# Performance work log

Hardware: AMD Instinct MI355X
Metric: run time of the kernel (lower is better)

The kernel has to match this reference:

```python
import jax, jax.numpy as jnp
import numpy as np


def setup_inputs() -> dict:
    key = jax.random.key(0)
    k1, k2 = jax.random.split(key)
    B, C, H, W, K = 8, 32, 224, 224, 5
    x = jax.random.normal(k1, (B, C, H, W), dtype=jnp.float32)
    kernel = jax.random.normal(k2, (C, 1, K, K), dtype=jnp.float32) * 0.1
    return {"x": x, "kernel": kernel, "stride": 1, "padding": 2, "dilation": 1}


def reference(x, kernel, stride, padding, dilation):
    # Tropical-max (morphological dilation) conv: out[p] = max_k (x[p+k] + w_flipped[k]).
    # is_max=True, softmax_temp=None -> hard max; kernel is flipped (true convolution).
    B, C, H, W = x.shape
    OC, _, K, _ = kernel.shape
    neutral = -jnp.inf
    x_pad = jnp.pad(x, ((0, 0), (0, 0), (padding, padding), (padding, padding)),
                    constant_values=neutral)
    Hp, Wp = H + 2 * padding, W + 2 * padding
    H_out = (Hp - dilation * (K - 1) - 1) // stride + 1
    W_out = (Wp - dilation * (K - 1) - 1) // stride + 1
    wflip = kernel[:, 0, ::-1, ::-1]  # (C, K, K) flipped, as in torch kernel.flip((2,3))
    # Start from neutral: matches the extra neutral row padded onto the unfold tensor.
    out = jnp.full((B, C, H_out, W_out), neutral, dtype=x.dtype)
    for i in range(K):  # small fixed K*K loop; avoids materializing the (B,C,K^2,HW) unfold
        for j in range(K):
            patch = x_pad[:, :,
                          i * dilation: i * dilation + (H_out - 1) * stride + 1: stride,
                          j * dilation: j * dilation + (W_out - 1) * stride + 1: stride]
            out = jnp.maximum(out, patch + wflip[:, i, j][None, :, None, None])
    return out
```

## Files before the change

### kernel.cpp

```cpp
#include <hip/hip_runtime.h>
#include <math.h>


#define TC_B 8
#define TC_C 32
#define TC_H 224
#define TC_W 224
#define TC_WQ (TC_W / 4)
#define TC_HG (TC_H / 16)
#define T_ROWS 20
#define T_STRIDE 240
#define T_F4_PER_ROW 56

__global__ __launch_bounds__(256) void tropical_conv2d_kernel(
    const float* __restrict__ x, const float* __restrict__ kern,
    float* __restrict__ out) {
  const int wq = threadIdx.x;
  const int hl = threadIdx.y;
  const int blk = blockIdx.x;
  const int hg = blk % TC_HG;
  const int bc = blk / TC_HG;
  const int c = bc % TC_C;

  __shared__ float tile[T_ROWS * T_STRIDE];

  const float NEG = -INFINITY;
  const float4 NINF4 = make_float4(NEG, NEG, NEG, NEG);
  const int t = hl * 64 + wq;
  const int row0 = hg * 16 - 2;
  const float* xp = x + (size_t)bc * (TC_H * TC_W);

  if (t < 40) {
    const int r = t % T_ROWS;
    const int cf = (t < T_ROWS) ? 0 : 57;
    *(float4*)&tile[r * T_STRIDE + cf * 4] = NINF4;
  }

  #pragma unroll
  for (int k = 0; k < 5; ++k) {
    const int idx = t + k * 256;
    if (idx < T_ROWS * T_F4_PER_ROW) {
      const int r = idx / T_F4_PER_ROW;
      const int cf = idx % T_F4_PER_ROW;
      const int ir = row0 + r;
      float4 val;
      if (ir >= 0 && ir < TC_H)
        val = ((const float4*)(xp + (size_t)ir * TC_W))[cf];
      else
        val = NINF4;
      *(float4*)&tile[r * T_STRIDE + (1 + cf) * 4] = val;
    }
  }

  float w[25];
  #pragma unroll
  for (int q = 0; q < 25; ++q) w[q] = kern[c * 25 + 24 - q];

  __syncthreads();

  if (wq >= TC_WQ) return;

  float acc[4][4];
  #pragma unroll
  for (int o = 0; o < 4; ++o)
    #pragma unroll
    for (int k = 0; k < 4; ++k) acc[o][k] = NEG;

  #pragma unroll
  for (int ri = 0; ri < 8; ++ri) {
    const float* rp = &tile[(hl * 4 + ri) * T_STRIDE + 4 * wq];
    const float4 A = *(const float4*)(rp);
    const float4 Bv = *(const float4*)(rp + 4);
    const float4 Cv = *(const float4*)(rp + 8);
    float v[12] = {A.x, A.y, A.z, A.w, Bv.x, Bv.y, Bv.z, Bv.w,
                   Cv.x, Cv.y, Cv.z, Cv.w};

    #pragma unroll
    for (int o = 0; o < 4; ++o) {
      const int i = ri - o;
      if (i < 0 || i > 4) continue;
      #pragma unroll
      for (int k = 0; k < 4; ++k) {
        const float t0 = v[2 + k + 0] + w[i * 5 + 0];
        const float t1 = v[2 + k + 1] + w[i * 5 + 1];
        const float t2 = v[2 + k + 2] + w[i * 5 + 2];
        const float t3 = v[2 + k + 3] + w[i * 5 + 3];
        const float t4 = v[2 + k + 4] + w[i * 5 + 4];
        acc[o][k] = fmaxf(fmaxf(fmaxf(acc[o][k], t0), t1),
                          fmaxf(fmaxf(t2, t3), t4));
      }
    }
  }

  float* op = out + (size_t)bc * (TC_H * TC_W) + (size_t)(hg * 16 + hl * 4) * TC_W;
  #pragma unroll
  for (int o = 0; o < 4; ++o) {
    ((float4*)(op + (size_t)o * TC_W))[wq] =
        make_float4(acc[o][0], acc[o][1], acc[o][2], acc[o][3]);
  }
}

extern "C" void kernel_launch(void* const* d_in, const int* in_sizes, int n_in,
                              void* d_out, int out_size, void* d_ws, size_t ws_size,
                              hipStream_t stream) {
  const float* x = (const float*)d_in[0];
  const float* k = (const float*)d_in[1];
  float* out = (float*)d_out;

  dim3 block(64, 4, 1);
  dim3 grid(TC_B * TC_C * TC_HG, 1, 1);
  tropical_conv2d_kernel<<<grid, block, 0, stream>>>(x, k, out);
}
```

Before: 114.8 us.

## Loop over row tiles per block with register-prefetched global loads

Each block now covers a quarter of an image plane (56 rows) instead of 16 rows. It walks four row tiles, prefetching the next tile's global data into registers while computing the current tile from shared memory. Blocks grow to 512 threads, with each thread producing 2 output rows instead of 4. The aim is to hide global load latency and amortise block launch and weight loads. In exchange there are fewer blocks, two barriers per tile, and more shared-memory reads per output.

After: 146.8 us. 27.9% more time.

```diff
diff --git a/kernel.cpp b/kernel.cpp
--- a/kernel.cpp
+++ b/kernel.cpp
@@ -6,97 +6,119 @@
 #define TC_C 32
 #define TC_H 224
 #define TC_W 224
-#define TC_WQ (TC_W / 4)
-#define TC_HG (TC_H / 16)
+#define TC_WQ 56
+#define T_STRIDE 232
 #define T_ROWS 20
-#define T_STRIDE 240
-#define T_F4_PER_ROW 56
+#define N_TILES 4
+#define QROWS 56
 
-__global__ __launch_bounds__(256) void tropical_conv2d_kernel(
+__global__ __launch_bounds__(512) void tropical_conv2d_kernel(
     const float* __restrict__ x, const float* __restrict__ kern,
     float* __restrict__ out) {
-  const int wq = threadIdx.x;
-  const int hl = threadIdx.y;
+  const int tt = threadIdx.x;
+  const int wq = tt & 63;
+  const int yl = tt >> 6;
   const int blk = blockIdx.x;
-  const int hg = blk % TC_HG;
-  const int bc = blk / TC_HG;
-  const int c = bc % TC_C;
+  const int hq = blk & 3;
+  const int bc = blk >> 2;
+  const int c = bc & (TC_C - 1);
+  const int h0 = hq * QROWS;
 
   __shared__ float tile[T_ROWS * T_STRIDE];
 
   const float NEG = -INFINITY;
   const float4 NINF4 = make_float4(NEG, NEG, NEG, NEG);
-  const int t = hl * 64 + wq;
-  const int row0 = hg * 16 - 2;
-  const float* xp = x + (size_t)bc * (TC_H * TC_W);
 
-  if (t < 40) {
-    const int r = t % T_ROWS;
-    const int cf = (t < T_ROWS) ? 0 : 57;
+  if (tt < 2 * T_ROWS) {
+    const int r = (tt >= T_ROWS) ? tt - T_ROWS : tt;
+    const int cf = (tt >= T_ROWS) ? 57 : 0;
     *(float4*)&tile[r * T_STRIDE + cf * 4] = NINF4;
-  }
-
-  #pragma unroll
-  for (int k = 0; k < 5; ++k) {
-    const int idx = t + k * 256;
-    if (idx < T_ROWS * T_F4_PER_ROW) {
-      const int r = idx / T_F4_PER_ROW;
-      const int cf = idx % T_F4_PER_ROW;
-      const int ir = row0 + r;
-      float4 val;
-      if (ir >= 0 && ir < TC_H)
-        val = ((const float4*)(xp + (size_t)ir * TC_W))[cf];
-      else
-        val = NINF4;
-      *(float4*)&tile[r * T_STRIDE + (1 + cf) * 4] = val;
-    }
   }
 
   float w[25];
   #pragma unroll
   for (int q = 0; q < 25; ++q) w[q] = kern[c * 25 + 24 - q];
 
-  __syncthreads();
+  const float* xp = x + (size_t)bc * (TC_H * TC_W);
+  float* op = out + (size_t)bc * (TC_H * TC_W);
 
-  if (wq >= TC_WQ) return;
+  int sr[3], sc[3];
+  bool sv[3];
+  #pragma unroll
+  for (int k = 0; k < 3; ++k) {
+    const int f = tt + k * 512;
+    sv[k] = f < T_ROWS * TC_WQ;
+    sr[k] = f / TC_WQ;
+    sc[k] = f % TC_WQ;
+  }
 
-  float acc[4][4];
+  float4 reg[3];
   #pragma unroll
-  for (int o = 0; o < 4; ++o)
+  for (int k = 0; k < 3; ++k) {
+    const int ir = h0 - 2 + sr[k];
+    reg[k] = (sv[k] && ir >= 0 && ir < TC_H)
+                 ? ((const float4*)(xp + (size_t)ir * TC_W))[sc[k]]
+                 : NINF4;
+  }
+
+  for (int t = 0; t < N_TILES; ++t) {
     #pragma unroll
-    for (int k = 0; k < 4; ++k) acc[o][k] = NEG;
+    for (int k = 0; k < 3; ++k)
+      if (sv[k]) *(float4*)&tile[sr[k] * T_STRIDE + 4 + 4 * sc[k]] = reg[k];
+    __syncthreads();
 
-  #pragma unroll
-  for (int ri = 0; ri < 8; ++ri) {
-    const float* rp = &tile[(hl * 4 + ri) * T_STRIDE + 4 * wq];
-    const float4 A = *(const float4*)(rp);
-    const float4 Bv = *(const float4*)(rp + 4);
-    const float4 Cv = *(const float4*)(rp + 8);
-    float v[12] = {A.x, A.y, A.z, A.w, Bv.x, Bv.y, Bv.z, Bv.w,
-                   Cv.x, Cv.y, Cv.z, Cv.w};
-
-    #pragma unroll
-    for (int o = 0; o < 4; ++o) {
-      const int i = ri - o;
-      if (i < 0 || i > 4) continue;
+    if (t + 1 < N_TILES) {
+      const int g0 = h0 + 16 * (t + 1) - 2;
       #pragma unroll
-      for (int k = 0; k < 4; ++k) {
-        const float t0 = v[2 + k + 0] + w[i * 5 + 0];
-        const float t1 = v[2 + k + 1] + w[i * 5 + 1];
-        const float t2 = v[2 + k + 2] + w[i * 5 + 2];
-        const float t3 = v[2 + k + 3] + w[i * 5 + 3];
-        const float t4 = v[2 + k + 4] + w[i * 5 + 4];
-        acc[o][k] = fmaxf(fmaxf(fmaxf(acc[o][k], t0), t1),
-                          fmaxf(fmaxf(t2, t3), t4));
+      for (int k = 0; k < 3; ++k) {
+        const int ir = g0 + sr[k];
+        reg[k] = (sv[k] && ir >= 0 && ir < TC_H)
+                     ? ((const float4*)(xp + (size_t)ir * TC_W))[sc[k]]
+                     : NINF4;
       }
     }
-  }
 
-  float* op = out + (size_t)bc * (TC_H * TC_W) + (size_t)(hg * 16 + hl * 4) * TC_W;
-  #pragma unroll
-  for (int o = 0; o < 4; ++o) {
-    ((float4*)(op + (size_t)o * TC_W))[wq] =
-        make_float4(acc[o][0], acc[o][1], acc[o][2], acc[o][3]);
+    const int nrows = (t < N_TILES - 1) ? 16 : 8;
+    const int tr0 = 2 * yl;
+    if (wq < TC_WQ && tr0 < nrows) {
+      float acc[2][4];
+      #pragma unroll
+      for (int o = 0; o < 2; ++o)
+        #pragma unroll
+        for (int k = 0; k < 4; ++k) acc[o][k] = NEG;
+
+      #pragma unroll
+      for (int jr = 0; jr < 6; ++jr) {
+        const float* rp = &tile[(tr0 + jr) * T_STRIDE + 4 * wq];
+        const float4 A = *(const float4*)(rp);
+        const float4 Bv = *(const float4*)(rp + 4);
+        const float4 Cv = *(const float4*)(rp + 8);
+        float v[12] = {A.x, A.y, A.z, A.w, Bv.x, Bv.y, Bv.z, Bv.w,
+                       Cv.x, Cv.y, Cv.z, Cv.w};
+        #pragma unroll
+        for (int o = 0; o < 2; ++o) {
+          const int i = jr - o;
+          if (i < 0 || i > 4) continue;
+          #pragma unroll
+          for (int k = 0; k < 4; ++k) {
+            const float t0 = v[2 + k] + w[i * 5 + 0];
+            const float t1 = v[3 + k] + w[i * 5 + 1];
+            const float t2 = v[4 + k] + w[i * 5 + 2];
+            const float t3 = v[5 + k] + w[i * 5 + 3];
+            const float t4 = v[6 + k] + w[i * 5 + 4];
+            acc[o][k] = fmaxf(fmaxf(fmaxf(acc[o][k], t0), t1),
+                              fmaxf(fmaxf(t2, t3), t4));
+          }
+        }
+      }
+
+      const int h = h0 + 16 * t + tr0;
+      ((float4*)(op + (size_t)h * TC_W))[wq] =
+          make_float4(acc[0][0], acc[0][1], acc[0][2], acc[0][3]);
+      ((float4*)(op + (size_t)(h + 1) * TC_W))[wq] =
+          make_float4(acc[1][0], acc[1][1], acc[1][2], acc[1][3]);
+    }
+    __syncthreads();
   }
 }
 
@@ -107,7 +129,7 @@
   const float* k = (const float*)d_in[1];
   float* out = (float*)d_out;
 
-  dim3 block(64, 4, 1);
-  dim3 grid(TC_B * TC_C * TC_HG, 1, 1);
+  dim3 block(512, 1, 1);
+  dim3 grid(TC_B * TC_C * 4, 1, 1);
   tropical_conv2d_kernel<<<grid, block, 0, stream>>>(x, k, out);
 }
```

## Replace shared-memory tile with direct per-thread global loads into registers

Applied to the files above, without the earlier changes.

Removes the LDS staging tile and __syncthreads. Each thread now loads its own 8 rows times 3 float4s (left, center, right neighbours) from global memory into registers, clamping indices and masking out-of-range values to -inf. This drops the shared-memory round trip and the barrier, but overlapping rows and neighbours are fetched redundantly from global and cache (about 24 loads per thread versus roughly 5 before). It also raises register pressure.

After: 118.8 us. 1.03x slower.

```diff
diff --git a/kernel.cpp b/kernel.cpp
--- a/kernel.cpp
+++ b/kernel.cpp
@@ -6,59 +6,58 @@
 #define TC_C 32
 #define TC_H 224
 #define TC_W 224
-#define TC_WQ (TC_W / 4)
-#define TC_HG (TC_H / 16)
-#define T_ROWS 20
-#define T_STRIDE 240
-#define T_F4_PER_ROW 56
+#define TC_WQ 56
+#define TC_HG 14
+
+__device__ __forceinline__ float4 sel4(bool ok, float4 v, float n) {
+  return make_float4(ok ? v.x : n, ok ? v.y : n, ok ? v.z : n, ok ? v.w : n);
+}
 
 __global__ __launch_bounds__(256) void tropical_conv2d_kernel(
     const float* __restrict__ x, const float* __restrict__ kern,
     float* __restrict__ out) {
-  const int wq = threadIdx.x;
-  const int hl = threadIdx.y;
+  const int tid = threadIdx.x;
+  const int wq = tid & 63;
+  const int yl = tid >> 6;
   const int blk = blockIdx.x;
   const int hg = blk % TC_HG;
   const int bc = blk / TC_HG;
-  const int c = bc % TC_C;
+  const int c = bc & (TC_C - 1);
 
-  __shared__ float tile[T_ROWS * T_STRIDE];
+  if (wq >= TC_WQ) return;
 
+  const int hbase = hg * 16 + yl * 4;
+  const float* xp = x + (size_t)bc * (TC_H * TC_W);
   const float NEG = -INFINITY;
-  const float4 NINF4 = make_float4(NEG, NEG, NEG, NEG);
-  const int t = hl * 64 + wq;
-  const int row0 = hg * 16 - 2;
-  const float* xp = x + (size_t)bc * (TC_H * TC_W);
 
-  if (t < 40) {
-    const int r = t % T_ROWS;
-    const int cf = (t < T_ROWS) ? 0 : 57;
-    *(float4*)&tile[r * T_STRIDE + cf * 4] = NINF4;
-  }
+  const int wqm1 = (wq > 0) ? wq - 1 : 0;
+  const int wqp1 = (wq < TC_WQ - 1) ? wq + 1 : TC_WQ - 1;
+  const bool lok = (wq > 0);
+  const bool rok = (wq < TC_WQ - 1);
 
+  float4 rA[8], rB[8], rC[8];
   #pragma unroll
-  for (int k = 0; k < 5; ++k) {
-    const int idx = t + k * 256;
-    if (idx < T_ROWS * T_F4_PER_ROW) {
-      const int r = idx / T_F4_PER_ROW;
-      const int cf = idx % T_F4_PER_ROW;
-      const int ir = row0 + r;
-      float4 val;
-      if (ir >= 0 && ir < TC_H)
-        val = ((const float4*)(xp + (size_t)ir * TC_W))[cf];
-      else
-        val = NINF4;
-      *(float4*)&tile[r * T_STRIDE + (1 + cf) * 4] = val;
-    }
+  for (int i = 0; i < 8; ++i) {
+    const int rr = hbase - 2 + i;
+    const int rc = rr < 0 ? 0 : (rr > TC_H - 1 ? TC_H - 1 : rr);
+    const float4* row = (const float4*)(xp + (size_t)rc * TC_W);
+    rA[i] = row[wqm1];
+    rB[i] = row[wq];
+    rC[i] = row[wqp1];
   }
 
   float w[25];
   #pragma unroll
   for (int q = 0; q < 25; ++q) w[q] = kern[c * 25 + 24 - q];
 
-  __syncthreads();
-
-  if (wq >= TC_WQ) return;
+  #pragma unroll
+  for (int i = 0; i < 8; ++i) {
+    const int rr = hbase - 2 + i;
+    const bool rowok = (rr >= 0) && (rr < TC_H);
+    rA[i] = sel4(rowok && lok, rA[i], NEG);
+    rB[i] = sel4(rowok, rB[i], NEG);
+    rC[i] = sel4(rowok && rok, rC[i], NEG);
+  }
 
   float acc[4][4];
   #pragma unroll
@@ -68,31 +67,27 @@
 
   #pragma unroll
   for (int ri = 0; ri < 8; ++ri) {
-    const float* rp = &tile[(hl * 4 + ri) * T_STRIDE + 4 * wq];
-    const float4 A = *(const float4*)(rp);
-    const float4 Bv = *(const float4*)(rp + 4);
-    const float4 Cv = *(const float4*)(rp + 8);
-    float v[12] = {A.x, A.y, A.z, A.w, Bv.x, Bv.y, Bv.z, Bv.w,
-                   Cv.x, Cv.y, Cv.z, Cv.w};
-
+    const float v[12] = {rA[ri].x, rA[ri].y, rA[ri].z, rA[ri].w,
+                         rB[ri].x, rB[ri].y, rB[ri].z, rB[ri].w,
+                         rC[ri].x, rC[ri].y, rC[ri].z, rC[ri].w};
     #pragma unroll
     for (int o = 0; o < 4; ++o) {
       const int i = ri - o;
       if (i < 0 || i > 4) continue;
       #pragma unroll
       for (int k = 0; k < 4; ++k) {
-        const float t0 = v[2 + k + 0] + w[i * 5 + 0];
-        const float t1 = v[2 + k + 1] + w[i * 5 + 1];
-        const float t2 = v[2 + k + 2] + w[i * 5 + 2];
-        const float t3 = v[2 + k + 3] + w[i * 5 + 3];
-        const float t4 = v[2 + k + 4] + w[i * 5 + 4];
+        const float t0 = v[2 + k] + w[i * 5 + 0];
+        const float t1 = v[3 + k] + w[i * 5 + 1];
+        const float t2 = v[4 + k] + w[i * 5 + 2];
+        const float t3 = v[5 + k] + w[i * 5 + 3];
+        const float t4 = v[6 + k] + w[i * 5 + 4];
         acc[o][k] = fmaxf(fmaxf(fmaxf(acc[o][k], t0), t1),
                           fmaxf(fmaxf(t2, t3), t4));
       }
     }
   }
 
-  float* op = out + (size_t)bc * (TC_H * TC_W) + (size_t)(hg * 16 + hl * 4) * TC_W;
+  float* op = out + (size_t)bc * (TC_H * TC_W) + (size_t)hbase * TC_W;
   #pragma unroll
   for (int o = 0; o < 4; ++o) {
     ((float4*)(op + (size_t)o * TC_W))[wq] =
@@ -107,7 +102,7 @@
   const float* k = (const float*)d_in[1];
   float* out = (float*)d_out;
 
-  dim3 block(64, 4, 1);
+  dim3 block(256, 1, 1);
   dim3 grid(TC_B * TC_C * TC_HG, 1, 1);
   tropical_conv2d_kernel<<<grid, block, 0, stream>>>(x, k, out);
 }
```
